# Kernel tuning notes

Hardware: AMD Instinct MI355X
Metric: run time of the kernel (lower is better)

Reference implementation:

```python
import jax, jax.numpy as jnp
import numpy as np

N = 100000
E = 1600000
IN_C = 128
HID = 128
NUM_CLASSES = 16


def setup_inputs() -> dict:
    key = jax.random.key(0)
    ks = jax.random.split(key, 8)
    x = jax.random.normal(ks[0], (N, IN_C), dtype=jnp.float32)
    edge_index = jax.random.randint(ks[1], (2, E), 0, N, dtype=jnp.int64)
    s1 = 1.0 / np.sqrt(IN_C)
    s2 = 1.0 / np.sqrt(HID)
    W1 = jax.random.uniform(ks[2], (IN_C, HID), jnp.float32, -s1, s1)
    b1 = jnp.zeros((HID,), jnp.float32)
    W2 = jax.random.uniform(ks[3], (HID, HID), jnp.float32, -s2, s2)
    b2 = jnp.zeros((HID,), jnp.float32)
    Wl = jax.random.uniform(ks[4], (HID, NUM_CLASSES), jnp.float32, -s2, s2)
    bl = jax.random.uniform(ks[5], (NUM_CLASSES,), jnp.float32, -s2, s2)
    return {"x": x, "edge_index": edge_index, "W1": W1, "b1": b1,
            "W2": W2, "b2": b2, "Wl": Wl, "bl": bl}


def gcn_conv(x, src, dst, norm, W, b, n_nodes):
    # x: [N, F_in]; src/dst: [E+N] (self-loops appended); norm: [E+N]
    h = x @ W  # [N, F_out] -- transform first (F_out <= F_in style), then gather
    msg = h[src] * norm[:, None]  # [E+N, F_out] gathered, normalized messages
    out = jax.ops.segment_sum(msg, dst, num_segments=n_nodes)  # scatter-add
    return out + b


def reference(x, edge_index, W1, b1, W2, b2, Wl, bl):
    loop = jnp.arange(N, dtype=edge_index.dtype)
    src = jnp.concatenate([edge_index[0], loop])  # add self-loops
    dst = jnp.concatenate([edge_index[1], loop])
    # symmetric GCN normalization: deg computed on target side incl. self-loops
    deg = jax.ops.segment_sum(jnp.ones_like(dst, dtype=x.dtype), dst,
                              num_segments=N)
    dinv = jnp.where(deg > 0, jax.lax.rsqrt(deg), 0.0)
    norm = dinv[src] * dinv[dst]  # [E+N]

    h = jax.nn.relu(gcn_conv(x, src, dst, norm, W1, b1, N))
    h = jax.nn.relu(gcn_conv(h, src, dst, norm, W2, b2, N))
    logits = h @ Wl + bl
    return jax.nn.softmax(logits, axis=1)
```

## Files before the change

### kernel.cpp

```cpp
#include <hip/hip_runtime.h>
#include <hip/hip_fp16.h>

#define FDIM 128
#define NCLS 16

#define SCAN_T 256
#define SCAN_I 8
#define SCAN_CHUNK (SCAN_T * SCAN_I)

#define EPB 4096
#define MAXBUK 64

typedef _Float16 f16x8 __attribute__((ext_vector_type(8)));
typedef float f32x4 __attribute__((ext_vector_type(4)));

__global__ void k_count(const int* __restrict__ dst, int* cnt, int e) {
    int i = blockIdx.x * blockDim.x + threadIdx.x;
    if (i < e) atomicAdd(&cnt[dst[i]], 1);
}

__global__ __launch_bounds__(SCAN_T) void k_scan1(const int* __restrict__ cnt,
                                                  int* __restrict__ excl,
                                                  int* __restrict__ blockSum,
                                                  float* __restrict__ dinv, int n) {
    __shared__ int ts[SCAN_T];
    int b = blockIdx.x, t = threadIdx.x;
    int base = b * SCAN_CHUNK + t * SCAN_I;
    int v[SCAN_I];
    int s = 0;
    #pragma unroll
    for (int i = 0; i < SCAN_I; ++i) {
        int idx = base + i;
        v[i] = (idx < n) ? cnt[idx] : 0;
        if (idx < n) dinv[idx] = rsqrtf((float)(v[i] + 1));
        s += v[i];
    }
    ts[t] = s;
    __syncthreads();
    for (int off = 1; off < SCAN_T; off <<= 1) {
        int x = (t >= off) ? ts[t - off] : 0;
        __syncthreads();
        ts[t] += x;
        __syncthreads();
    }
    int ex = (t == 0) ? 0 : ts[t - 1];
    #pragma unroll
    for (int i = 0; i < SCAN_I; ++i) {
        int idx = base + i;
        if (idx < n) excl[idx] = ex;
        ex += v[i];
    }
    if (t == SCAN_T - 1) blockSum[b] = ts[SCAN_T - 1];
}

__global__ __launch_bounds__(1024) void k_scan2_prepw(int* blockSum, int* total, int nb,
                                                      const float* __restrict__ W1,
                                                      const float* __restrict__ W2,
                                                      __half* __restrict__ T1,
                                                      __half* __restrict__ T2) {
    if (blockIdx.x == 0) {
        __shared__ int ts[1024];
        int t = threadIdx.x;
        int v = (t < nb) ? blockSum[t] : 0;
        ts[t] = v;
        __syncthreads();
        for (int off = 1; off < 1024; off <<= 1) {
            int x = (t >= off) ? ts[t - off] : 0;
            __syncthreads();
            ts[t] += x;
            __syncthreads();
        }
        if (t < nb) blockSum[t] = (t == 0) ? 0 : ts[t - 1];
        if (t == 1023) *total = ts[1023];
    } else {
        const float* W = (blockIdx.x == 1) ? W1 : W2;
        __half* T = (blockIdx.x == 1) ? T1 : T2;
        for (int i = threadIdx.x; i < 128 * 32; i += 1024) {
            int c = i >> 5, k4 = (i & 31) * 4;
            float a = W[(k4 + 0) * 128 + c];
            float b = W[(k4 + 1) * 128 + c];
            float d = W[(k4 + 2) * 128 + c];
            float f = W[(k4 + 3) * 128 + c];
            __half2 h0 = __float22half2_rn(make_float2(a, b));
            __half2 h1 = __float22half2_rn(make_float2(d, f));
            uint2 u;
            u.x = *reinterpret_cast<unsigned int*>(&h0);
            u.y = *reinterpret_cast<unsigned int*>(&h1);
            *reinterpret_cast<uint2*>(&T[c * 128 + k4]) = u;
        }
    }
}

__global__ void k_scan3(int* __restrict__ row_ptr, int* __restrict__ cursor,
                        const int* __restrict__ blockSum, const int* __restrict__ total,
                        int* __restrict__ bcur, int shift, int n) {
    int i = blockIdx.x * blockDim.x + threadIdx.x;
    if (i < n) {
        int v = row_ptr[i] + blockSum[i / SCAN_CHUNK];
        row_ptr[i] = v;
        cursor[i] = v;
        if ((i & ((1 << shift) - 1)) == 0) bcur[i >> shift] = v;
    }
    if (i == 0) row_ptr[n] = *total;
}

__global__ __launch_bounds__(512) void k_bucket(const int* __restrict__ src,
                                                const int* __restrict__ dst,
                                                int* bcur, uint2* __restrict__ pairs,
                                                int e, int shift, int nbuk) {
    __shared__ int hist[MAXBUK], lhist[MAXBUK], base[MAXBUK], lpre[MAXBUK];
    __shared__ uint2 slab[EPB];
    __shared__ unsigned char bkt[EPB];
    int t = threadIdx.x;
    int e0 = blockIdx.x * EPB;
    int cntE = min(EPB, e - e0);

    if (t < nbuk) { hist[t] = 0; lhist[t] = 0; }
    __syncthreads();

    for (int k = t; k < cntE; k += 512) {
        int b = dst[e0 + k] >> shift;
        atomicAdd(&hist[b], 1);
    }
    __syncthreads();

    if (t < nbuk) base[t] = atomicAdd(&bcur[t], hist[t]);
    if (t == 0) {
        int acc = 0;
        for (int b = 0; b < nbuk; ++b) { lpre[b] = acc; acc += hist[b]; }
    }
    __syncthreads();

    for (int k = t; k < cntE; k += 512) {
        int d = dst[e0 + k];
        int s = src[e0 + k];
        int b = d >> shift;
        int r = atomicAdd(&lhist[b], 1);
        int j = lpre[b] + r;
        slab[j] = make_uint2((unsigned)(s << 8), (unsigned)d);
        bkt[j] = (unsigned char)b;
    }
    __syncthreads();

    for (int j = t; j < cntE; j += 512) {
        int b = bkt[j];
        pairs[base[b] + (j - lpre[b])] = slab[j];
    }
}

__global__ void k_fine(const uint2* __restrict__ pairs, int* cursor,
                       int* __restrict__ csr_off, int e) {
    int i = blockIdx.x * blockDim.x + threadIdx.x;
    if (i >= e) return;
    uint2 up = pairs[i];
    int pos = atomicAdd(&cursor[up.y], 1);
    csr_off[pos] = (int)up.x;
}

template <typename T>
__global__ __launch_bounds__(512) void k_gemm_mfma(const T* __restrict__ A,
                                                   const __half* __restrict__ WT,
                                                   const float* __restrict__ dinv,
                                                   __half* __restrict__ C, int n) {
    __shared__ _Float16 as[128 * 128];
    __shared__ _Float16 wt[128 * 128];
    int t = threadIdx.x;
    int r0 = blockIdx.x * 128;

    for (int i = t; i < 2048; i += 512) {
        int c = i >> 4, k8 = i & 15;
        uint4 u = reinterpret_cast<const uint4*>(WT)[i];
        int byte = (c * 256 + k8 * 16) ^ ((c & 7) << 4);
        *reinterpret_cast<uint4*>(reinterpret_cast<char*>(wt) + byte) = u;
    }

    if constexpr (sizeof(T) == 4) {
        for (int i = t; i < 128 * 16; i += 512) {
            int r = i >> 4, c8 = i & 15;
            float4 v0 = make_float4(0.f, 0.f, 0.f, 0.f);
            float4 v1 = make_float4(0.f, 0.f, 0.f, 0.f);
            if (r0 + r < n) {
                v0 = reinterpret_cast<const float4*>(A)[(size_t)(r0 + r) * 32 + c8 * 2];
                v1 = reinterpret_cast<const float4*>(A)[(size_t)(r0 + r) * 32 + c8 * 2 + 1];
            }
            __half2 h0 = __float22half2_rn(make_float2(v0.x, v0.y));
            __half2 h1 = __float22half2_rn(make_float2(v0.z, v0.w));
            __half2 h2 = __float22half2_rn(make_float2(v1.x, v1.y));
            __half2 h3 = __float22half2_rn(make_float2(v1.z, v1.w));
            uint4 u;
            u.x = *reinterpret_cast<unsigned int*>(&h0);
            u.y = *reinterpret_cast<unsigned int*>(&h1);
            u.z = *reinterpret_cast<unsigned int*>(&h2);
            u.w = *reinterpret_cast<unsigned int*>(&h3);
            int byte = (r * 256 + c8 * 16) ^ ((r & 7) << 4);
            *reinterpret_cast<uint4*>(reinterpret_cast<char*>(as) + byte) = u;
        }
    } else {
        for (int i = t; i < 128 * 16; i += 512) {
            int r = i >> 4, c8 = i & 15;
            uint4 u = make_uint4(0, 0, 0, 0);
            if (r0 + r < n)
                u = reinterpret_cast<const uint4*>(A)[(size_t)(r0 + r) * 16 + c8];
            int byte = (r * 256 + c8 * 16) ^ ((r & 7) << 4);
            *reinterpret_cast<uint4*>(reinterpret_cast<char*>(as) + byte) = u;
        }
    }
    __syncthreads();

    int w = t >> 6, l = t & 63;
    int lrow = l & 15, lk = l >> 4;
    int rw = w * 16;

    f16x8 afrag[4];
    #pragma unroll
    for (int ks = 0; ks < 4; ++ks) {
        int row = rw + lrow;
        int byte = (row * 256 + (ks * 4 + lk) * 16) ^ ((row & 7) << 4);
        afrag[ks] = *reinterpret_cast<const f16x8*>(reinterpret_cast<const char*>(as) + byte);
    }
    float dv[4];
    #pragma unroll
    for (int reg = 0; reg < 4; ++reg) {
        int rg = r0 + rw + lk * 4 + reg;
        dv[reg] = (rg < n) ? dinv[rg] : 0.f;
    }

    #pragma unroll
    for (int ct = 0; ct < 8; ++ct) {
        f32x4 acc = {0.f, 0.f, 0.f, 0.f};
        #pragma unroll
        for (int ks = 0; ks < 4; ++ks) {
            int c = ct * 16 + lrow;
            int byte = (c * 256 + (ks * 4 + lk) * 16) ^ ((c & 7) << 4);
            f16x8 bfrag = *reinterpret_cast<const f16x8*>(reinterpret_cast<const char*>(wt) + byte);
            acc = __builtin_amdgcn_mfma_f32_16x16x32_f16(afrag[ks], bfrag, acc, 0, 0, 0);
        }
        #pragma unroll
        for (int reg = 0; reg < 4; ++reg) {
            int rg = r0 + rw + lk * 4 + reg;
            if (rg < n)
                C[(size_t)rg * FDIM + ct * 16 + lrow] = __float2half(acc[reg] * dv[reg]);
        }
    }
}

template <bool FUSE>
__global__ __launch_bounds__(256) void k_agg2e(const __half* __restrict__ Y,
                                               const int* __restrict__ csr_off,
                                               const int* __restrict__ row_ptr,
                                               const float* __restrict__ dinv,
                                               const float* __restrict__ bias,
                                               const float* __restrict__ Wl,
                                               const float* __restrict__ bl,
                                               __half* __restrict__ hout,
                                               float* __restrict__ out, int n) {
    __shared__ float s_wl[NCLS * FDIM];
    __shared__ float s_bl[NCLS];
    if (FUSE) {
        for (int i = threadIdx.x; i < FDIM * NCLS / 4; i += 256) {
            int k = i >> 2, c4 = (i & 3) * 4;
            float4 v = reinterpret_cast<const float4*>(Wl)[i];
            s_wl[(c4 + 0) * FDIM + k] = v.x;
            s_wl[(c4 + 1) * FDIM + k] = v.y;
            s_wl[(c4 + 2) * FDIM + k] = v.z;
            s_wl[(c4 + 3) * FDIM + k] = v.w;
        }
        if (threadIdx.x < NCLS) s_bl[threadIdx.x] = bl[threadIdx.x];
        __syncthreads();
    }

    int node = blockIdx.x * 4 + (threadIdx.x >> 6);
    if (node >= n) return;
    int lane = threadIdx.x & 63;
    int half = lane >> 5, l32 = lane & 31;
    const char* Yb = reinterpret_cast<const char*>(Y);
    const char* lanebase = Yb + (l32 << 3);

    float a0 = 0.f, a1 = 0.f, a2 = 0.f, a3 = 0.f;
    int beg = row_ptr[node], end = row_ptr[node + 1];

    for (int j0 = beg; j0 < end; j0 += 64) {
        int cnt = min(64, end - j0);
        int myoff = (j0 + lane < end) ? csr_off[j0 + lane] : 0;
        int k = 0;
        for (; k + 8 <= cnt; k += 8) {
            uint2 u[4];
            #pragma unroll
            for (int i = 0; i < 4; ++i) {
                int oe = __builtin_amdgcn_readlane(myoff, k + 2 * i);
                int oo = __builtin_amdgcn_readlane(myoff, k + 2 * i + 1);
                int off = half ? oo : oe;
                u[i] = *reinterpret_cast<const uint2*>(lanebase + off);
            }
            __half2* p = reinterpret_cast<__half2*>(u);
            __half2 lo = __hadd2(__hadd2(p[0], p[2]), __hadd2(p[4], p[6]));
            __half2 hi = __hadd2(__hadd2(p[1], p[3]), __hadd2(p[5], p[7]));
            float2 flo = __half22float2(lo), fhi = __half22float2(hi);
            a0 += flo.x; a1 += flo.y; a2 += fhi.x; a3 += fhi.y;
        }
        for (; k + 2 <= cnt; k += 2) {
            int oe = __builtin_amdgcn_readlane(myoff, k);
            int oo = __builtin_amdgcn_readlane(myoff, k + 1);
            int off = half ? oo : oe;
            uint2 u = *reinterpret_cast<const uint2*>(lanebase + off);
            __half2* p = reinterpret_cast<__half2*>(&u);
            float2 flo = __half22float2(p[0]), fhi = __half22float2(p[1]);
            a0 += flo.x; a1 += flo.y; a2 += fhi.x; a3 += fhi.y;
        }
        if (k < cnt) {
            int o = __builtin_amdgcn_readlane(myoff, k);
            uint2 u = *reinterpret_cast<const uint2*>(lanebase + o);
            __half2* p = reinterpret_cast<__half2*>(&u);
            float sel = (half == 0) ? 1.0f : 0.0f;
            float2 flo = __half22float2(p[0]), fhi = __half22float2(p[1]);
            a0 += flo.x * sel; a1 += flo.y * sel;
            a2 += fhi.x * sel; a3 += fhi.y * sel;
        }
    }

    a0 += __shfl_xor(a0, 32, 64);
    a1 += __shfl_xor(a1, 32, 64);
    a2 += __shfl_xor(a2, 32, 64);
    a3 += __shfl_xor(a3, 32, 64);

    uint2 su = *reinterpret_cast<const uint2*>(Yb + ((size_t)node << 8) + (l32 << 3));
    __half2* sp = reinterpret_cast<__half2*>(&su);
    float2 slo = __half22float2(sp[0]), shi = __half22float2(sp[1]);
    a0 += slo.x; a1 += slo.y; a2 += shi.x; a3 += shi.y;

    float di = dinv[node];
    float4 b = *reinterpret_cast<const float4*>(bias + l32 * 4);
    float h0 = fmaxf(a0 * di + b.x, 0.f);
    float h1 = fmaxf(a1 * di + b.y, 0.f);
    float h2 = fmaxf(a2 * di + b.z, 0.f);
    float h3 = fmaxf(a3 * di + b.w, 0.f);

    if (!FUSE) {
        if (half == 0) {
            __half2 o0 = __float22half2_rn(make_float2(h0, h1));
            __half2 o1 = __float22half2_rn(make_float2(h2, h3));
            uint2 o;
            o.x = *reinterpret_cast<unsigned int*>(&o0);
            o.y = *reinterpret_cast<unsigned int*>(&o1);
            *reinterpret_cast<uint2*>(reinterpret_cast<char*>(hout) + ((size_t)node << 8) + (l32 << 3)) = o;
        }
    } else {
        float lg[NCLS];
        #pragma unroll
        for (int c = 0; c < NCLS; ++c) {
            float4 w4 = *reinterpret_cast<const float4*>(&s_wl[c * FDIM + l32 * 4]);
            lg[c] = h0 * w4.x + h1 * w4.y + h2 * w4.z + h3 * w4.w;
        }
        #pragma unroll
        for (int off = 1; off < 32; off <<= 1) {
            #pragma unroll
            for (int c = 0; c < NCLS; ++c) lg[c] += __shfl_xor(lg[c], off, 64);
        }
        #pragma unroll
        for (int c = 0; c < NCLS; ++c) lg[c] += s_bl[c];
        float m = lg[0];
        #pragma unroll
        for (int c = 1; c < NCLS; ++c) m = fmaxf(m, lg[c]);
        float ev[NCLS];
        float sum = 0.f;
        #pragma unroll
        for (int c = 0; c < NCLS; ++c) { ev[c] = __expf(lg[c] - m); sum += ev[c]; }
        float inv = 1.0f / sum;
        float mye = 0.f;
        #pragma unroll
        for (int c = 0; c < NCLS; ++c) if (lane == c) mye = ev[c];
        if (lane < NCLS) out[(size_t)node * NCLS + lane] = mye * inv;
    }
}

extern "C" void kernel_launch(void* const* d_in, const int* in_sizes, int n_in,
                              void* d_out, int out_size, void* d_ws, size_t ws_size,
                              hipStream_t stream) {
    const float* x  = (const float*)d_in[0];
    const int*   ei = (const int*)d_in[1];
    const float* W1 = (const float*)d_in[2];
    const float* b1 = (const float*)d_in[3];
    const float* W2 = (const float*)d_in[4];
    const float* b2 = (const float*)d_in[5];
    const float* Wl = (const float*)d_in[6];
    const float* bl = (const float*)d_in[7];
    float* out = (float*)d_out;

    int n = in_sizes[0] / FDIM;
    int e = in_sizes[1] / 2;
    const int* src = ei;
    const int* dst = ei + e;

    int nb = (n + SCAN_CHUNK - 1) / SCAN_CHUNK;

    int shift = 11;
    while (((n + (1 << shift) - 1) >> shift) > MAXBUK) ++shift;
    int nbuk = (n + (1 << shift) - 1) >> shift;

    float* dinv    = (float*)d_ws;
    int*   cnt     = (int*)(dinv + n);
    int*   row_ptr = cnt + n;
    int*   cursor  = row_ptr + n + 1;
    int*   blockSum= cursor + n;
    int*   total   = blockSum + 1024;
    int*   bcur    = total + 1;
    int*   csr_off = bcur + MAXBUK;
    uintptr_t p = (uintptr_t)(csr_off + e);
    p = (p + 15) & ~(uintptr_t)15;
    uint2* pairs = (uint2*)p;
    __half* wt1 = (__half*)(pairs + e);
    __half* wt2 = wt1 + 128 * 128;
    __half* bufA = wt2 + 128 * 128;
    __half* bufB = bufA + (size_t)n * FDIM;

    int bn = (n + 255) / 256;
    int be = (e + 255) / 256;

    hipMemsetAsync(cnt, 0, (size_t)n * sizeof(int), stream);
    k_count<<<be, 256, 0, stream>>>(dst, cnt, e);
    k_scan1<<<nb, SCAN_T, 0, stream>>>(cnt, row_ptr, blockSum, dinv, n);
    k_scan2_prepw<<<3, 1024, 0, stream>>>(blockSum, total, nb, W1, W2, wt1, wt2);
    k_scan3<<<bn, 256, 0, stream>>>(row_ptr, cursor, blockSum, total, bcur, shift, n);

    int bbk = (e + EPB - 1) / EPB;
    k_bucket<<<bbk, 512, 0, stream>>>(src, dst, bcur, pairs, e, shift, nbuk);
    k_fine<<<be, 256, 0, stream>>>(pairs, cursor, csr_off, e);

    int bg = (n + 127) / 128;
    int ba = (n + 3) / 4;

    k_gemm_mfma<float><<<bg, 512, 0, stream>>>(x, wt1, dinv, bufA, n);
    k_agg2e<false><<<ba, 256, 0, stream>>>(bufA, csr_off, row_ptr, dinv, b1, Wl, bl, bufB, out, n);

    k_gemm_mfma<__half><<<bg, 512, 0, stream>>>(bufB, wt2, dinv, bufA, n);
    k_agg2e<true><<<ba, 256, 0, stream>>>(bufA, csr_off, row_ptr, dinv, b2, Wl, bl, bufB, out, n);
}
```

Baseline: 421.4 us.

## Schedule aggregation nodes in descending-degree order via a degree-binned permutation

Builds a histogram of in-degrees (capped at 64 bins) during the scan, prefix-sums it, and produces a permutation that lists nodes from highest to lowest degree. Both aggregation kernels now map each wavefront to perm[gid], so waves with similar edge counts run together and heavy nodes start first, which is meant to reduce load imbalance and tail effects. The cost is extra atomics in the scan kernels, one more indirection per wave, and a loss of locality in node order when writing outputs.

```diff
diff --git a/kernel.cpp b/kernel.cpp
--- a/kernel.cpp
+++ b/kernel.cpp
@@ -10,6 +10,7 @@
 
 #define EPB 4096
 #define MAXBUK 64
+#define DBINS 64
 
 typedef _Float16 f16x8 __attribute__((ext_vector_type(8)));
 typedef float f32x4 __attribute__((ext_vector_type(4)));
@@ -22,9 +23,14 @@
 __global__ __launch_bounds__(SCAN_T) void k_scan1(const int* __restrict__ cnt,
                                                   int* __restrict__ excl,
                                                   int* __restrict__ blockSum,
-                                                  float* __restrict__ dinv, int n) {
+                                                  float* __restrict__ dinv,
+                                                  int* __restrict__ dbase, int n) {
     __shared__ int ts[SCAN_T];
+    __shared__ int dh[DBINS];
     int b = blockIdx.x, t = threadIdx.x;
+    if (t < DBINS) dh[t] = 0;
+    __syncthreads();
+
     int base = b * SCAN_CHUNK + t * SCAN_I;
     int v[SCAN_I];
     int s = 0;
@@ -32,11 +38,15 @@
     for (int i = 0; i < SCAN_I; ++i) {
         int idx = base + i;
         v[i] = (idx < n) ? cnt[idx] : 0;
-        if (idx < n) dinv[idx] = rsqrtf((float)(v[i] + 1));
+        if (idx < n) {
+            dinv[idx] = rsqrtf((float)(v[i] + 1));
+            atomicAdd(&dh[(DBINS - 1) - min(v[i], DBINS - 1)], 1);
+        }
         s += v[i];
     }
     ts[t] = s;
     __syncthreads();
+    if (t < DBINS && dh[t]) atomicAdd(&dbase[t], dh[t]);
     for (int off = 1; off < SCAN_T; off <<= 1) {
         int x = (t >= off) ? ts[t - off] : 0;
         __syncthreads();
@@ -54,6 +64,7 @@
 }
 
 __global__ __launch_bounds__(1024) void k_scan2_prepw(int* blockSum, int* total, int nb,
+                                                      int* __restrict__ dbase,
                                                       const float* __restrict__ W1,
                                                       const float* __restrict__ W2,
                                                       __half* __restrict__ T1,
@@ -72,6 +83,10 @@
         }
         if (t < nb) blockSum[t] = (t == 0) ? 0 : ts[t - 1];
         if (t == 1023) *total = ts[1023];
+        if (t == 0) {
+            int acc = 0;
+            for (int b = 0; b < DBINS; ++b) { int c = dbase[b]; dbase[b] = acc; acc += c; }
+        }
     } else {
         const float* W = (blockIdx.x == 1) ? W1 : W2;
         __half* T = (blockIdx.x == 1) ? T1 : T2;
@@ -91,17 +106,34 @@
     }
 }
 
-__global__ void k_scan3(int* __restrict__ row_ptr, int* __restrict__ cursor,
-                        const int* __restrict__ blockSum, const int* __restrict__ total,
-                        int* __restrict__ bcur, int shift, int n) {
-    int i = blockIdx.x * blockDim.x + threadIdx.x;
+__global__ __launch_bounds__(256) void k_scan3(int* __restrict__ row_ptr,
+                                               int* __restrict__ cursor,
+                                               const int* __restrict__ blockSum,
+                                               const int* __restrict__ total,
+                                               int* __restrict__ bcur, int shift,
+                                               const int* __restrict__ cnt,
+                                               int* __restrict__ dcur,
+                                               int* __restrict__ perm, int n) {
+    __shared__ int lh[DBINS], lbase[DBINS];
+    int t = threadIdx.x;
+    if (t < DBINS) lh[t] = 0;
+    __syncthreads();
+
+    int i = blockIdx.x * 256 + t;
+    int mybin = 0, myrank = 0;
     if (i < n) {
         int v = row_ptr[i] + blockSum[i / SCAN_CHUNK];
         row_ptr[i] = v;
         cursor[i] = v;
         if ((i & ((1 << shift) - 1)) == 0) bcur[i >> shift] = v;
+        mybin = (DBINS - 1) - min(cnt[i], DBINS - 1);
+        myrank = atomicAdd(&lh[mybin], 1);
     }
     if (i == 0) row_ptr[n] = *total;
+    __syncthreads();
+    if (t < DBINS) lbase[t] = lh[t] ? atomicAdd(&dcur[t], lh[t]) : 0;
+    __syncthreads();
+    if (i < n) perm[lbase[mybin] + myrank] = i;
 }
 
 __global__ __launch_bounds__(512) void k_bucket(const int* __restrict__ src,
@@ -248,6 +280,7 @@
 __global__ __launch_bounds__(256) void k_agg2e(const __half* __restrict__ Y,
                                                const int* __restrict__ csr_off,
                                                const int* __restrict__ row_ptr,
+                                               const int* __restrict__ perm,
                                                const float* __restrict__ dinv,
                                                const float* __restrict__ bias,
                                                const float* __restrict__ Wl,
@@ -269,8 +302,9 @@
         __syncthreads();
     }
 
-    int node = blockIdx.x * 4 + (threadIdx.x >> 6);
-    if (node >= n) return;
+    int gid = blockIdx.x * 4 + (threadIdx.x >> 6);
+    if (gid >= n) return;
+    int node = perm[gid];
     int lane = threadIdx.x & 63;
     int half = lane >> 5, l32 = lane & 31;
     const char* Yb = reinterpret_cast<const char*>(Y);
@@ -399,9 +433,11 @@
 
     float* dinv    = (float*)d_ws;
     int*   cnt     = (int*)(dinv + n);
-    int*   row_ptr = cnt + n;
+    int*   dbase   = cnt + n;
+    int*   row_ptr = dbase + DBINS;
     int*   cursor  = row_ptr + n + 1;
-    int*   blockSum= cursor + n;
+    int*   perm    = cursor + n;
+    int*   blockSum= perm + n;
     int*   total   = blockSum + 1024;
     int*   bcur    = total + 1;
     int*   csr_off = bcur + MAXBUK;
@@ -416,11 +452,12 @@
     int bn = (n + 255) / 256;
     int be = (e + 255) / 256;
 
-    hipMemsetAsync(cnt, 0, (size_t)n * sizeof(int), stream);
+    hipMemsetAsync(cnt, 0, (size_t)(n + DBINS) * sizeof(int), stream);
     k_count<<<be, 256, 0, stream>>>(dst, cnt, e);
-    k_scan1<<<nb, SCAN_T, 0, stream>>>(cnt, row_ptr, blockSum, dinv, n);
-    k_scan2_prepw<<<3, 1024, 0, stream>>>(blockSum, total, nb, W1, W2, wt1, wt2);
-    k_scan3<<<bn, 256, 0, stream>>>(row_ptr, cursor, blockSum, total, bcur, shift, n);
+    k_scan1<<<nb, SCAN_T, 0, stream>>>(cnt, row_ptr, blockSum, dinv, dbase, n);
+    k_scan2_prepw<<<3, 1024, 0, stream>>>(blockSum, total, nb, dbase, W1, W2, wt1, wt2);
+    k_scan3<<<bn, 256, 0, stream>>>(row_ptr, cursor, blockSum, total, bcur, shift,
+                                    cnt, dbase, perm, n);
 
     int bbk = (e + EPB - 1) / EPB;
     k_bucket<<<bbk, 512, 0, stream>>>(src, dst, bcur, pairs, e, shift, nbuk);
@@ -430,8 +467,8 @@
     int ba = (n + 3) / 4;
 
     k_gemm_mfma<float><<<bg, 512, 0, stream>>>(x, wt1, dinv, bufA, n);
-    k_agg2e<false><<<ba, 256, 0, stream>>>(bufA, csr_off, row_ptr, dinv, b1, Wl, bl, bufB, out, n);
+    k_agg2e<false><<<ba, 256, 0, stream>>>(bufA, csr_off, row_ptr, perm, dinv, b1, Wl, bl, bufB, out, n);
 
     k_gemm_mfma<__half><<<bg, 512, 0, stream>>>(bufB, wt2, dinv, bufA, n);
-    k_agg2e<true><<<ba, 256, 0, stream>>>(bufA, csr_off, row_ptr, dinv, b2, Wl, bl, bufB, out, n);
-}
+    k_agg2e<true><<<ba, 256, 0, stream>>>(bufA, csr_off, row_ptr, perm, dinv, b2, Wl, bl, bufB, out, n);
+}
```

Result: slower. 431.8 us (+2.5%).
